# Performance work log

Measured on AMD Instinct MI355X. Metric: run time of the kernel, lower is better.

The kernel has to match this reference:

```python
import jax, jax.numpy as jnp
import numpy as np

T, B, C = 1024, 8, 256
H, F = 8, 512
D = C // H  # head dim = 32
EPS = 1e-5


def _layernorm(x, g, b):
    mu = jnp.mean(x, axis=-1, keepdims=True)
    var = jnp.var(x, axis=-1, keepdims=True)
    return (x - mu) * jax.lax.rsqrt(var + EPS) * g + b


def setup_inputs() -> dict:
    key = jax.random.key(0)
    ks = jax.random.split(key, 12)
    s = 0.02
    return {
        "x_TBC": jax.random.normal(ks[0], (T, B, C), jnp.float32),
        "key_padding_mask": jnp.zeros((B, T), dtype=bool),
        "edge_bias": jax.random.normal(ks[1], (B, H, T, T), jnp.float32),
        "ln1_g": jnp.ones((C,), jnp.float32),
        "ln1_b": jnp.zeros((C,), jnp.float32),
        "ln2_g": jnp.ones((C,), jnp.float32),
        "ln2_b": jnp.zeros((C,), jnp.float32),
        "w_qkv": jax.random.normal(ks[2], (3 * C, C), jnp.float32) * s,
        "b_qkv": jnp.zeros((3 * C,), jnp.float32),
        "w_o": jax.random.normal(ks[3], (C, C), jnp.float32) * s,
        "b_o": jnp.zeros((C,), jnp.float32),
        "w1": jax.random.normal(ks[4], (F, C), jnp.float32) * s,
        "b1": jnp.zeros((F,), jnp.float32),
        "w2": jax.random.normal(ks[5], (C, F), jnp.float32) * s,
        "b2": jnp.zeros((C,), jnp.float32),
    }


def _attn(y, key_padding_mask, edge_bias, w_qkv, b_qkv, w_o, b_o):
    # y: [T,B,C]
    qkv = jnp.einsum('tbc,ec->tbe', y, w_qkv) + b_qkv  # [T,B,3C]
    q, k, v = jnp.split(qkv, 3, axis=-1)
    def heads(z):  # [T,B,C] -> [B,H,T,D]
        return z.reshape(T, B, H, D).transpose(1, 2, 0, 3)
    q, k, v = heads(q), heads(k), heads(v)
    scale = 1.0 / jnp.sqrt(jnp.asarray(D, jnp.float32))
    scores = jnp.einsum('bhqd,bhkd->bhqk', q * scale, k) + edge_bias
    neg = jnp.asarray(-1e9, scores.dtype)
    scores = jnp.where(key_padding_mask[:, None, None, :], neg, scores)
    probs = jax.nn.softmax(scores, axis=-1)
    o = jnp.einsum('bhqk,bhkd->bhqd', probs, v)  # [B,H,T,D]
    o = o.transpose(2, 0, 1, 3).reshape(T, B, C)
    return jnp.einsum('tbc,ec->tbe', o, w_o) + b_o


def reference(x_TBC, key_padding_mask, edge_bias, ln1_g, ln1_b, ln2_g, ln2_b,
              w_qkv, b_qkv, w_o, b_o, w1, b1, w2, b2):
    # pre-LN: LN -> attn(edge bias) -> residual, LN -> FFN -> residual
    y = _layernorm(x_TBC, ln1_g, ln1_b)
    y = _attn(y, key_padding_mask, edge_bias, w_qkv, b_qkv, w_o, b_o)
    x = x_TBC + y
    y = _layernorm(x, ln2_g, ln2_b)
    y = jax.nn.gelu(jnp.einsum('tbc,fc->tbf', y, w1) + b1, approximate=False)
    y = jnp.einsum('tbf,cf->tbc', y, w2) + b2
    return x + y
```

## Files before the change

kernel.cpp:

```cpp
#include <hip/hip_runtime.h>
#include <hip/hip_bf16.h>
#include <cmath>

#define T_DIM 1024
#define B_DIM 8
#define C_DIM 256
#define H_DIM 8
#define D_DIM 32
#define F_DIM 512

typedef __attribute__((ext_vector_type(4))) float f32x4;
typedef __attribute__((ext_vector_type(8))) short bf16x8;

static __device__ __forceinline__ unsigned short f2bf(float f) {
    union { float f; unsigned u; } v; v.f = f;
    unsigned r = v.u + 0x7fff + ((v.u >> 16) & 1);
    return (unsigned short)(r >> 16);
}
static __device__ __forceinline__ float bf2f(unsigned short h) {
    union { unsigned u; float f; } v; v.u = ((unsigned)h) << 16;
    return v.f;
}

static __device__ __forceinline__ void gload_lds16(const void* g, void* l) {
    __builtin_amdgcn_global_load_lds(
        (const __attribute__((address_space(1))) unsigned int*)g,
        (__attribute__((address_space(3))) unsigned int*)l,
        16, 0, 0);
}

__global__ __launch_bounds__(256) void convert_weights(const float* __restrict__ wqkv,
                                                       const float* __restrict__ wo,
                                                       const float* __restrict__ w1,
                                                       const float* __restrict__ w2,
                                                       unsigned short* __restrict__ dst)
{
    int e = blockIdx.x * 256 + threadIdx.x;
    const float* src; int off;
    if (e < 196608)      { src = wqkv; off = 0; }
    else if (e < 262144) { src = wo;   off = 196608; }
    else if (e < 393216) { src = w1;   off = 262144; }
    else                 { src = w2;   off = 393216; }
    dst[e] = f2bf(src[e - off]);
}

__global__ __launch_bounds__(256) void ln_bf16(const float* __restrict__ x,
                                               const float* __restrict__ g,
                                               const float* __restrict__ bta,
                                               unsigned short* __restrict__ y)
{
    int row  = blockIdx.x * 4 + (threadIdx.x >> 6);
    int lane = threadIdx.x & 63;
    float4 v = ((const float4*)(x + (size_t)row * C_DIM))[lane];
    float s  = v.x + v.y + v.z + v.w;
    float ss = v.x * v.x + v.y * v.y + v.z * v.z + v.w * v.w;
#pragma unroll
    for (int off = 1; off < 64; off <<= 1) {
        s  += __shfl_xor(s, off);
        ss += __shfl_xor(ss, off);
    }
    float mu   = s * (1.0f / C_DIM);
    float var  = ss * (1.0f / C_DIM) - mu * mu;
    float rstd = rsqrtf(var + 1e-5f);
    float4 gv = ((const float4*)g)[lane];
    float4 bv = ((const float4*)bta)[lane];
    ushort4 o;
    o.x = f2bf((v.x - mu) * rstd * gv.x + bv.x);
    o.y = f2bf((v.y - mu) * rstd * gv.y + bv.y);
    o.z = f2bf((v.z - mu) * rstd * gv.z + bv.z);
    o.w = f2bf((v.w - mu) * rstd * gv.w + bv.w);
    ((ushort4*)(y + (size_t)row * C_DIM))[lane] = o;
}

__global__ __launch_bounds__(256) void ln_bf16i(const unsigned short* __restrict__ x,
                                                const float* __restrict__ g,
                                                const float* __restrict__ bta,
                                                unsigned short* __restrict__ y)
{
    int row  = blockIdx.x * 4 + (threadIdx.x >> 6);
    int lane = threadIdx.x & 63;
    ushort4 hv = ((const ushort4*)(x + (size_t)row * C_DIM))[lane];
    float4 v = {bf2f(hv.x), bf2f(hv.y), bf2f(hv.z), bf2f(hv.w)};
    float s  = v.x + v.y + v.z + v.w;
    float ss = v.x * v.x + v.y * v.y + v.z * v.z + v.w * v.w;
#pragma unroll
    for (int off = 1; off < 64; off <<= 1) {
        s  += __shfl_xor(s, off);
        ss += __shfl_xor(ss, off);
    }
    float mu   = s * (1.0f / C_DIM);
    float var  = ss * (1.0f / C_DIM) - mu * mu;
    float rstd = rsqrtf(var + 1e-5f);
    float4 gv = ((const float4*)g)[lane];
    float4 bv = ((const float4*)bta)[lane];
    ushort4 o;
    o.x = f2bf((v.x - mu) * rstd * gv.x + bv.x);
    o.y = f2bf((v.y - mu) * rstd * gv.y + bv.y);
    o.z = f2bf((v.z - mu) * rstd * gv.z + bv.z);
    o.w = f2bf((v.w - mu) * rstd * gv.w + bv.w);
    ((ushort4*)(y + (size_t)row * C_DIM))[lane] = o;
}

template<int EPI>
__global__ __launch_bounds__(256) void gemm_mfma(const unsigned short* __restrict__ A,
                                                 const unsigned short* __restrict__ W,
                                                 const float* __restrict__ bias,
                                                 const void* __restrict__ Rv,
                                                 void* __restrict__ outv,
                                                 int N, int K)
{
    __shared__ __align__(16) unsigned short A_s[128 * 64];
    __shared__ __align__(16) unsigned short W_s[64 * 64];
    int tid  = threadIdx.x;
    int lane = tid & 63;
    int wv   = tid >> 6;
    int l15  = lane & 15, lg = lane >> 4;
    int row0 = blockIdx.y * 128;
    int col0 = blockIdx.x * 64;

    f32x4 acc[2][4] = {};
    for (int k0 = 0; k0 < K; k0 += 64) {
#pragma unroll
        for (int i = 0; i < 4; i++) {
            int u = (wv * 4 + i) * 64 + lane;
            int r = u >> 3, c = u & 7;
            gload_lds16(A + (size_t)(row0 + r) * K + k0 + ((c ^ (r & 7)) * 8),
                        &A_s[(size_t)(wv * 4 + i) * 512]);
        }
#pragma unroll
        for (int j = 0; j < 2; j++) {
            int u = (wv * 2 + j) * 64 + lane;
            int r = u >> 3, c = u & 7;
            gload_lds16(W + (size_t)(col0 + r) * K + k0 + ((c ^ (r & 7)) * 8),
                        &W_s[(size_t)(wv * 2 + j) * 512]);
        }
        __syncthreads();
#pragma unroll
        for (int kk = 0; kk < 2; kk++) {
            bf16x8 af[2], wf[4];
#pragma unroll
            for (int mb = 0; mb < 2; mb++) {
                int rowa = wv * 32 + mb * 16 + l15;
                af[mb] = *(const bf16x8*)&A_s[rowa * 64 + (((kk * 4 + lg) ^ (l15 & 7)) * 8)];
            }
#pragma unroll
            for (int nb = 0; nb < 4; nb++) {
                int roww = nb * 16 + l15;
                wf[nb] = *(const bf16x8*)&W_s[roww * 64 + (((kk * 4 + lg) ^ (l15 & 7)) * 8)];
            }
#pragma unroll
            for (int mb = 0; mb < 2; mb++)
#pragma unroll
                for (int nb = 0; nb < 4; nb++)
                    acc[mb][nb] = __builtin_amdgcn_mfma_f32_16x16x32_bf16(af[mb], wf[nb], acc[mb][nb], 0, 0, 0);
        }
        __syncthreads();
    }
#pragma unroll
    for (int nb = 0; nb < 4; nb++) {
        int c = col0 + nb * 16 + l15;
        float bv = bias[c];
#pragma unroll
        for (int mb = 0; mb < 2; mb++) {
#pragma unroll
            for (int r = 0; r < 4; r++) {
                int rowm = row0 + wv * 32 + mb * 16 + lg * 4 + r;
                float v = acc[mb][nb][r] + bv;
                if (EPI == 4) {
                    unsigned short* qh = (unsigned short*)outv;
                    unsigned short* kh = qh + 2097152;
                    unsigned short* vt = qh + 4194304;
                    int t  = rowm >> 3, b_ = rowm & 7;
                    int h  = (c >> 5) & 7, d = c & 31;
                    int bh = b_ * 8 + h;
                    if (c < 256)      qh[(size_t)bh * 32768 + t * 32 + d] = f2bf(v);
                    else if (c < 512) kh[(size_t)bh * 32768 + t * 32 + d] = f2bf(v);
                    else              vt[(size_t)bh * 32768 + d * 1024 + t] = f2bf(v);
                } else if (EPI == 3) {
                    v += bf2f(((const unsigned short*)Rv)[(size_t)rowm * N + c]);
                    ((float*)outv)[(size_t)rowm * N + c] = v;
                } else {
                    if (EPI == 1) v = 0.5f * v * (1.0f + erff(v * 0.70710678118654752f));
                    if (EPI == 2) v += ((const float*)Rv)[(size_t)rowm * N + c];
                    ((unsigned short*)outv)[(size_t)rowm * N + c] = f2bf(v);
                }
            }
        }
    }
}

__global__ __launch_bounds__(256, 4) void attn_mfma(const unsigned short* __restrict__ Qh,
                                                    const unsigned short* __restrict__ Kh,
                                                    const unsigned short* __restrict__ Vt,
                                                    const float* __restrict__ bias,
                                                    const unsigned char* __restrict__ mask,
                                                    unsigned short* __restrict__ o)
{
    __shared__ __align__(16) float bias_lds[2][4][1024];
    __shared__ unsigned short P_s[4][16][64];

    int tid  = threadIdx.x;
    int lane = tid & 63;
    int wv   = tid >> 6;
    int l15  = lane & 15, lg = lane >> 4;
    int bid  = blockIdx.x;
    int bh   = (bid & 7) + (bid >> 7) * 8;
    int qg   = (bid >> 3) & 15;
    int b    = bh >> 3, hh = bh & 7;
    int q0   = qg * 64 + wv * 16;
    const float scale = 0.17677669529663687f;

    const unsigned short* kbase = Kh + (size_t)bh * 32768;
    const unsigned short* vbase = Vt + (size_t)bh * 32768;

    bf16x8 qf = *(const bf16x8*)(Qh + (size_t)bh * 32768 + (q0 + l15) * 32 + lg * 8);
    const unsigned char* mptr = mask + (size_t)b * T_DIM + lg * 4;
    int swz = (l15 & 7) << 3;

    int gq = lane >> 2, gj = lane & 3;
    const float* bsrc = bias + ((size_t)bh * T_DIM + q0 + gq) * T_DIM + gj * 4;

    float m_run = -INFINITY, l_run = 0.0f;
    f32x4 oacc[2] = {};

#pragma unroll
    for (int p = 0; p < 4; p++)
        gload_lds16(bsrc + p * 16, &bias_lds[0][wv][p * 256]);
    __syncthreads();

    for (int t = 0; t < 16; t++) {
        int k0  = t << 6;
        int buf = t & 1;

        if (t < 15) {
#pragma unroll
            for (int p = 0; p < 4; p++)
                gload_lds16(bsrc + (t + 1) * 64 + p * 16, &bias_lds[buf ^ 1][wv][p * 256]);
        }

        bf16x8 kf[4];
        uint32_t mw[4];
#pragma unroll
        for (int kb = 0; kb < 4; kb++) {
            kf[kb] = *(const bf16x8*)(kbase + (size_t)(k0 + kb * 16 + l15) * 32 + lg * 8);
            mw[kb] = *(const uint32_t*)(mptr + k0 + kb * 16);
        }

        float sv[4][4];
        float tmax = -INFINITY;
        __builtin_amdgcn_s_setprio(1);
#pragma unroll
        for (int kb = 0; kb < 4; kb++) {
            f32x4 z = {0.0f, 0.0f, 0.0f, 0.0f};
            f32x4 sc = __builtin_amdgcn_mfma_f32_16x16x32_bf16(kf[kb], qf, z, 0, 0, 0);
            f32x4 bv = *(const f32x4*)&bias_lds[buf][wv][kb * 256 + l15 * 16 + lg * 4];
#pragma unroll
            for (int r = 0; r < 4; r++) {
                float s = sc[r] * scale + bv[r];
                if ((mw[kb] >> (8 * r)) & 0xff) s = -1e9f;
                sv[kb][r] = s;
                tmax = fmaxf(tmax, s);
            }
        }
        __builtin_amdgcn_s_setprio(0);

        bf16x8 vf[2][2];
#pragma unroll
        for (int h = 0; h < 2; h++)
#pragma unroll
            for (int db = 0; db < 2; db++)
                vf[h][db] = *(const bf16x8*)(vbase + (size_t)(db * 16 + l15) * 1024
                                             + k0 + h * 32 + lg * 8);

        tmax = fmaxf(tmax, __shfl_xor(tmax, 16));
        tmax = fmaxf(tmax, __shfl_xor(tmax, 32));
        float m_new = fmaxf(m_run, tmax);
        float corr = __expf(m_run - m_new);
        m_run = m_new;

        float ls = 0.0f;
#pragma unroll
        for (int kb = 0; kb < 4; kb++) {
            float p0 = __expf(sv[kb][0] - m_new);
            float p1 = __expf(sv[kb][1] - m_new);
            float p2 = __expf(sv[kb][2] - m_new);
            float p3 = __expf(sv[kb][3] - m_new);
            ls += (p0 + p1) + (p2 + p3);
            uint2 pw;
            pw.x = (uint32_t)f2bf(p0) | ((uint32_t)f2bf(p1) << 16);
            pw.y = (uint32_t)f2bf(p2) | ((uint32_t)f2bf(p3) << 16);
            *(uint2*)&P_s[wv][l15][(kb * 16 + lg * 4) ^ swz] = pw;
        }
        ls += __shfl_xor(ls, 16);
        ls += __shfl_xor(ls, 32);
        l_run = l_run * corr + ls;
#pragma unroll
        for (int db = 0; db < 2; db++)
#pragma unroll
            for (int r = 0; r < 4; r++) oacc[db][r] *= corr;

        __builtin_amdgcn_s_setprio(1);
#pragma unroll
        for (int h = 0; h < 2; h++) {
            bf16x8 pf = *(const bf16x8*)&P_s[wv][l15][(h * 32 + lg * 8) ^ swz];
#pragma unroll
            for (int db = 0; db < 2; db++)
                oacc[db] = __builtin_amdgcn_mfma_f32_16x16x32_bf16(vf[h][db], pf, oacc[db], 0, 0, 0);
        }
        __builtin_amdgcn_s_setprio(0);

        __syncthreads();
    }

    float inv = 1.0f / l_run;
#pragma unroll
    for (int db = 0; db < 2; db++) {
        ushort4 ov;
        ov.x = f2bf(oacc[db][0] * inv);
        ov.y = f2bf(oacc[db][1] * inv);
        ov.z = f2bf(oacc[db][2] * inv);
        ov.w = f2bf(oacc[db][3] * inv);
        *(ushort4*)(o + ((size_t)(q0 + l15) * B_DIM + b) * C_DIM + hh * 32 + db * 16 + lg * 4) = ov;
    }
}

extern "C" void kernel_launch(void* const* d_in, const int* in_sizes, int n_in,
                              void* d_out, int out_size, void* d_ws, size_t ws_size,
                              hipStream_t stream)
{
    const float* x            = (const float*)d_in[0];
    const unsigned char* mask = (const unsigned char*)d_in[1];
    const float* bias         = (const float*)d_in[2];
    const float* ln1g         = (const float*)d_in[3];
    const float* ln1b         = (const float*)d_in[4];
    const float* ln2g         = (const float*)d_in[5];
    const float* ln2b         = (const float*)d_in[6];
    const float* wqkv         = (const float*)d_in[7];
    const float* bqkv         = (const float*)d_in[8];
    const float* wo           = (const float*)d_in[9];
    const float* bo           = (const float*)d_in[10];
    const float* w1           = (const float*)d_in[11];
    const float* b1           = (const float*)d_in[12];
    const float* w2           = (const float*)d_in[13];
    const float* b2           = (const float*)d_in[14];
    float* out = (float*)d_out;
    char* ws   = (char*)d_ws;

    unsigned short* wbf     = (unsigned short*)ws;
    unsigned short* wqkv_bf = wbf;
    unsigned short* wo_bf   = wbf + 196608;
    unsigned short* w1_bf   = wbf + 262144;
    unsigned short* w2_bf   = wbf + 393216;
    unsigned short* y_bf    = (unsigned short*)(ws + (1u << 20));
    unsigned short* qkvs    = (unsigned short*)(ws + 5u * (1u << 20));
    unsigned short* o_bf    = (unsigned short*)(ws + 17u * (1u << 20));
    unsigned short* x1_bf   = (unsigned short*)(ws + 21u * (1u << 20));
    unsigned short* h_bf    = (unsigned short*)(ws + 29u * (1u << 20));

    unsigned short* Qh = qkvs;
    unsigned short* Kh = qkvs + 2097152;
    unsigned short* Vt = qkvs + 4194304;

    const int M = T_DIM * B_DIM;

    convert_weights<<<2048, 256, 0, stream>>>(wqkv, wo, w1, w2, wbf);
    ln_bf16<<<M / 4, 256, 0, stream>>>(x, ln1g, ln1b, y_bf);
    gemm_mfma<4><<<dim3(768 / 64, M / 128), 256, 0, stream>>>(y_bf, wqkv_bf, bqkv, nullptr, qkvs, 768, 256);
    attn_mfma<<<1024, 256, 0, stream>>>(Qh, Kh, Vt, bias, mask, o_bf);
    gemm_mfma<2><<<dim3(256 / 64, M / 128), 256, 0, stream>>>(o_bf, wo_bf, bo, x, x1_bf, 256, 256);
    ln_bf16i<<<M / 4, 256, 0, stream>>>(x1_bf, ln2g, ln2b, y_bf);
    gemm_mfma<1><<<dim3(512 / 64, M / 128), 256, 0, stream>>>(y_bf, w1_bf, b1, nullptr, h_bf, 512, 256);
    gemm_mfma<3><<<dim3(256 / 64, M / 128), 256, 0, stream>>>(h_bf, w2_bf, b2, x1_bf, out, 256, 512);
}
```

Measured before the change: 139.0 us.

## Stage K, V, mask and bf16 bias in LDS with register-prefetched 256-key chunks

The attention kernel now loads 256-key chunks of K, V and the edge bias into registers one stage ahead, then writes them to padded LDS (bias converted to bf16). Each chunk is shared by the block's four waves and consumed over four 64-key tiles, replacing per-wave global loads of K/V/mask on every tile. This cuts redundant global traffic and the number of barriers, but raises register and LDS use (launch bounds lowered to 2 blocks per CU). Rounding the bias to bf16 also slightly reduces accuracy.

```diff
diff --git a/kernel.cpp b/kernel.cpp
--- a/kernel.cpp
+++ b/kernel.cpp
@@ -20,6 +20,12 @@
 static __device__ __forceinline__ float bf2f(unsigned short h) {
     union { unsigned u; float f; } v; v.u = ((unsigned)h) << 16;
     return v.f;
+}
+static __device__ __forceinline__ float bflo(uint32_t w) {
+    union { unsigned u; float f; } v; v.u = w << 16; return v.f;
+}
+static __device__ __forceinline__ float bfhi(uint32_t w) {
+    union { unsigned u; float f; } v; v.u = w & 0xffff0000u; return v.f;
 }
 
 static __device__ __forceinline__ void gload_lds16(const void* g, void* l) {
@@ -189,14 +195,17 @@
     }
 }
 
-__global__ __launch_bounds__(256, 4) void attn_mfma(const unsigned short* __restrict__ Qh,
+__global__ __launch_bounds__(256, 2) void attn_mfma(const unsigned short* __restrict__ Qh,
                                                     const unsigned short* __restrict__ Kh,
                                                     const unsigned short* __restrict__ Vt,
                                                     const float* __restrict__ bias,
                                                     const unsigned char* __restrict__ mask,
                                                     unsigned short* __restrict__ o)
 {
-    __shared__ __align__(16) float bias_lds[2][4][1024];
+    __shared__ __align__(16) unsigned short bias_s[64][276];
+    __shared__ __align__(16) unsigned short K_s[256 * 36];
+    __shared__ __align__(16) unsigned short V_s[32 * 260];
+    __shared__ unsigned char m_s[1024];
     __shared__ unsigned short P_s[4][16][64];
 
     int tid  = threadIdx.x;
@@ -207,109 +216,153 @@
     int bh   = (bid & 7) + (bid >> 7) * 8;
     int qg   = (bid >> 3) & 15;
     int b    = bh >> 3, hh = bh & 7;
-    int q0   = qg * 64 + wv * 16;
+    int q0b  = qg * 64;
+    int qw   = q0b + wv * 16;
     const float scale = 0.17677669529663687f;
 
-    const unsigned short* kbase = Kh + (size_t)bh * 32768;
-    const unsigned short* vbase = Vt + (size_t)bh * 32768;
-
-    bf16x8 qf = *(const bf16x8*)(Qh + (size_t)bh * 32768 + (q0 + l15) * 32 + lg * 8);
-    const unsigned char* mptr = mask + (size_t)b * T_DIM + lg * 4;
+    bf16x8 qf = *(const bf16x8*)(Qh + (size_t)bh * 32768 + (qw + l15) * 32 + lg * 8);
     int swz = (l15 & 7) << 3;
 
-    int gq = lane >> 2, gj = lane & 3;
-    const float* bsrc = bias + ((size_t)bh * T_DIM + q0 + gq) * T_DIM + gj * 4;
+    int brow = tid >> 2, bhq = tid & 3;
+    const float* bp0 = bias + ((size_t)bh * T_DIM + q0b + brow) * T_DIM + bhq * 32;
+    const unsigned short* kp0 = Kh + (size_t)bh * 32768 + tid * 32;
+    const unsigned short* vp0 = Vt + (size_t)bh * 32768 + (tid >> 3) * 1024 + (tid & 7) * 32;
+
+    f32x4 bst[2][8];
+    uint4 kst[4], vst[4];
+
+#define ATTN_ISSUE(SN)                                                          \
+    {                                                                           \
+        const float* bp = bp0 + (SN) * 256;                                     \
+        _Pragma("unroll")                                                       \
+        for (int h = 0; h < 2; h++)                                             \
+            _Pragma("unroll")                                                   \
+            for (int i = 0; i < 8; i++)                                         \
+                bst[h][i] = *(const f32x4*)(bp + h * 128 + i * 4);              \
+        const unsigned short* kp = kp0 + (size_t)(SN) * 256 * 32;               \
+        _Pragma("unroll")                                                       \
+        for (int i = 0; i < 4; i++) kst[i] = *(const uint4*)(kp + i * 8);       \
+        const unsigned short* vp = vp0 + (SN) * 256;                            \
+        _Pragma("unroll")                                                       \
+        for (int i = 0; i < 4; i++) vst[i] = *(const uint4*)(vp + i * 8);       \
+    }
+
+#define ATTN_WRITE()                                                            \
+    {                                                                           \
+        _Pragma("unroll")                                                       \
+        for (int h = 0; h < 2; h++) {                                           \
+            int qtr = 2 * h + (bhq >> 1);                                       \
+            unsigned short* dst = &bias_s[brow][qtr * 68 + (bhq & 1) * 32];     \
+            _Pragma("unroll")                                                   \
+            for (int i = 0; i < 8; i++) {                                       \
+                uint2 w;                                                        \
+                w.x = (uint32_t)f2bf(bst[h][i][0]) | ((uint32_t)f2bf(bst[h][i][1]) << 16); \
+                w.y = (uint32_t)f2bf(bst[h][i][2]) | ((uint32_t)f2bf(bst[h][i][3]) << 16); \
+                *(uint2*)(dst + i * 4) = w;                                     \
+            }                                                                   \
+        }                                                                       \
+        _Pragma("unroll")                                                       \
+        for (int i = 0; i < 4; i++) {                                           \
+            *(uint2*)&K_s[tid * 36 + i * 8]     = make_uint2(kst[i].x, kst[i].y); \
+            *(uint2*)&K_s[tid * 36 + i * 8 + 4] = make_uint2(kst[i].z, kst[i].w); \
+        }                                                                       \
+        int vrow = tid >> 3, vseg = tid & 7;                                    \
+        _Pragma("unroll")                                                       \
+        for (int i = 0; i < 4; i++) {                                           \
+            *(uint2*)&V_s[vrow * 260 + vseg * 32 + i * 8]     = make_uint2(vst[i].x, vst[i].y); \
+            *(uint2*)&V_s[vrow * 260 + vseg * 32 + i * 8 + 4] = make_uint2(vst[i].z, vst[i].w); \
+        }                                                                       \
+    }
+
+    *(uint32_t*)&m_s[tid * 4] = *(const uint32_t*)(mask + (size_t)b * T_DIM + tid * 4);
+    ATTN_ISSUE(0);
+    ATTN_WRITE();
+    __syncthreads();
 
     float m_run = -INFINITY, l_run = 0.0f;
     f32x4 oacc[2] = {};
 
-#pragma unroll
-    for (int p = 0; p < 4; p++)
-        gload_lds16(bsrc + p * 16, &bias_lds[0][wv][p * 256]);
-    __syncthreads();
-
-    for (int t = 0; t < 16; t++) {
-        int k0  = t << 6;
-        int buf = t & 1;
-
-        if (t < 15) {
-#pragma unroll
-            for (int p = 0; p < 4; p++)
-                gload_lds16(bsrc + (t + 1) * 64 + p * 16, &bias_lds[buf ^ 1][wv][p * 256]);
-        }
-
-        bf16x8 kf[4];
-        uint32_t mw[4];
-#pragma unroll
-        for (int kb = 0; kb < 4; kb++) {
-            kf[kb] = *(const bf16x8*)(kbase + (size_t)(k0 + kb * 16 + l15) * 32 + lg * 8);
-            mw[kb] = *(const uint32_t*)(mptr + k0 + kb * 16);
-        }
-
-        float sv[4][4];
-        float tmax = -INFINITY;
-        __builtin_amdgcn_s_setprio(1);
-#pragma unroll
-        for (int kb = 0; kb < 4; kb++) {
-            f32x4 z = {0.0f, 0.0f, 0.0f, 0.0f};
-            f32x4 sc = __builtin_amdgcn_mfma_f32_16x16x32_bf16(kf[kb], qf, z, 0, 0, 0);
-            f32x4 bv = *(const f32x4*)&bias_lds[buf][wv][kb * 256 + l15 * 16 + lg * 4];
-#pragma unroll
-            for (int r = 0; r < 4; r++) {
-                float s = sc[r] * scale + bv[r];
-                if ((mw[kb] >> (8 * r)) & 0xff) s = -1e9f;
-                sv[kb][r] = s;
-                tmax = fmaxf(tmax, s);
-            }
-        }
-        __builtin_amdgcn_s_setprio(0);
-
-        bf16x8 vf[2][2];
-#pragma unroll
-        for (int h = 0; h < 2; h++)
+    union U8 { uint4 u; bf16x8 v; };
+
+    for (int S = 0; S < 4; S++) {
+        if (S < 3) ATTN_ISSUE(S + 1);
+
+        for (int kt = 0; kt < 4; kt++) {
+            int k0l = kt * 64;
+            int k0g = S * 256 + k0l;
+
+            float sv[4][4];
+            float tmax = -INFINITY;
+            __builtin_amdgcn_s_setprio(1);
+#pragma unroll
+            for (int kb = 0; kb < 4; kb++) {
+                int krow = (k0l + kb * 16 + l15) * 36 + lg * 8;
+                uint2 ka = *(const uint2*)&K_s[krow];
+                uint2 kb2 = *(const uint2*)&K_s[krow + 4];
+                U8 kt_u; kt_u.u = make_uint4(ka.x, ka.y, kb2.x, kb2.y);
+                f32x4 z = {0.0f, 0.0f, 0.0f, 0.0f};
+                f32x4 sc = __builtin_amdgcn_mfma_f32_16x16x32_bf16(kt_u.v, qf, z, 0, 0, 0);
+                uint2 bw = *(const uint2*)&bias_s[wv * 16 + l15][kt * 68 + kb * 16 + lg * 4];
+                float bv[4] = {bflo(bw.x), bfhi(bw.x), bflo(bw.y), bfhi(bw.y)};
+                uint32_t mw = *(const uint32_t*)&m_s[k0g + kb * 16 + lg * 4];
+#pragma unroll
+                for (int r = 0; r < 4; r++) {
+                    float s = sc[r] * scale + bv[r];
+                    if ((mw >> (8 * r)) & 0xff) s = -1e9f;
+                    sv[kb][r] = s;
+                    tmax = fmaxf(tmax, s);
+                }
+            }
+            __builtin_amdgcn_s_setprio(0);
+
+            tmax = fmaxf(tmax, __shfl_xor(tmax, 16));
+            tmax = fmaxf(tmax, __shfl_xor(tmax, 32));
+            float m_new = fmaxf(m_run, tmax);
+            float corr = __expf(m_run - m_new);
+            m_run = m_new;
+
+            float ls = 0.0f;
+#pragma unroll
+            for (int kb = 0; kb < 4; kb++) {
+                float p0 = __expf(sv[kb][0] - m_new);
+                float p1 = __expf(sv[kb][1] - m_new);
+                float p2 = __expf(sv[kb][2] - m_new);
+                float p3 = __expf(sv[kb][3] - m_new);
+                ls += (p0 + p1) + (p2 + p3);
+                uint2 pw;
+                pw.x = (uint32_t)f2bf(p0) | ((uint32_t)f2bf(p1) << 16);
+                pw.y = (uint32_t)f2bf(p2) | ((uint32_t)f2bf(p3) << 16);
+                *(uint2*)&P_s[wv][l15][(kb * 16 + lg * 4) ^ swz] = pw;
+            }
+            ls += __shfl_xor(ls, 16);
+            ls += __shfl_xor(ls, 32);
+            l_run = l_run * corr + ls;
 #pragma unroll
             for (int db = 0; db < 2; db++)
-                vf[h][db] = *(const bf16x8*)(vbase + (size_t)(db * 16 + l15) * 1024
-                                             + k0 + h * 32 + lg * 8);
-
-        tmax = fmaxf(tmax, __shfl_xor(tmax, 16));
-        tmax = fmaxf(tmax, __shfl_xor(tmax, 32));
-        float m_new = fmaxf(m_run, tmax);
-        float corr = __expf(m_run - m_new);
-        m_run = m_new;
-
-        float ls = 0.0f;
-#pragma unroll
-        for (int kb = 0; kb < 4; kb++) {
-            float p0 = __expf(sv[kb][0] - m_new);
-            float p1 = __expf(sv[kb][1] - m_new);
-            float p2 = __expf(sv[kb][2] - m_new);
-            float p3 = __expf(sv[kb][3] - m_new);
-            ls += (p0 + p1) + (p2 + p3);
-            uint2 pw;
-            pw.x = (uint32_t)f2bf(p0) | ((uint32_t)f2bf(p1) << 16);
-            pw.y = (uint32_t)f2bf(p2) | ((uint32_t)f2bf(p3) << 16);
-            *(uint2*)&P_s[wv][l15][(kb * 16 + lg * 4) ^ swz] = pw;
-        }
-        ls += __shfl_xor(ls, 16);
-        ls += __shfl_xor(ls, 32);
-        l_run = l_run * corr + ls;
-#pragma unroll
-        for (int db = 0; db < 2; db++)
-#pragma unroll
-            for (int r = 0; r < 4; r++) oacc[db][r] *= corr;
-
-        __builtin_amdgcn_s_setprio(1);
-#pragma unroll
-        for (int h = 0; h < 2; h++) {
-            bf16x8 pf = *(const bf16x8*)&P_s[wv][l15][(h * 32 + lg * 8) ^ swz];
-#pragma unroll
-            for (int db = 0; db < 2; db++)
-                oacc[db] = __builtin_amdgcn_mfma_f32_16x16x32_bf16(vf[h][db], pf, oacc[db], 0, 0, 0);
-        }
-        __builtin_amdgcn_s_setprio(0);
+#pragma unroll
+                for (int r = 0; r < 4; r++) oacc[db][r] *= corr;
+
+            __builtin_amdgcn_s_setprio(1);
+#pragma unroll
+            for (int h = 0; h < 2; h++) {
+                bf16x8 pf = *(const bf16x8*)&P_s[wv][l15][(h * 32 + lg * 8) ^ swz];
+#pragma unroll
+                for (int db = 0; db < 2; db++) {
+                    int voff = (db * 16 + l15) * 260 + k0l + h * 32 + lg * 8;
+                    uint2 va = *(const uint2*)&V_s[voff];
+                    uint2 vb = *(const uint2*)&V_s[voff + 4];
+                    U8 vt_u; vt_u.u = make_uint4(va.x, va.y, vb.x, vb.y);
+                    oacc[db] = __builtin_amdgcn_mfma_f32_16x16x32_bf16(vt_u.v, pf, oacc[db], 0, 0, 0);
+                }
+            }
+            __builtin_amdgcn_s_setprio(0);
+        }
 
         __syncthreads();
+        if (S < 3) {
+            ATTN_WRITE();
+            __syncthreads();
+        }
     }
 
     float inv = 1.0f / l_run;
@@ -320,8 +373,10 @@
         ov.y = f2bf(oacc[db][1] * inv);
         ov.z = f2bf(oacc[db][2] * inv);
         ov.w = f2bf(oacc[db][3] * inv);
-        *(ushort4*)(o + ((size_t)(q0 + l15) * B_DIM + b) * C_DIM + hh * 32 + db * 16 + lg * 4) = ov;
-    }
+        *(ushort4*)(o + ((size_t)(qw + l15) * B_DIM + b) * C_DIM + hh * 32 + db * 16 + lg * 4) = ov;
+    }
+#undef ATTN_ISSUE
+#undef ATTN_WRITE
 }
 
 extern "C" void kernel_launch(void* const* d_in, const int* in_sizes, int n_in,
```

After: 143.4 us. 3.2% more time.
